# Kernel optimization log

Hardware: AMD Instinct MI355X
Metric: run time of the kernel (lower is better)

Reference implementation:

```python
import jax, jax.numpy as jnp
import numpy as np

N_HEADS = 4
N_NODES = 10000
EMB = 128
N_BATCH = 4096
N_NEAREST = 8
N_SENTINELS = 8


def setup_inputs() -> dict:
    key = jax.random.key(0)
    k1, k2, k3, k4 = jax.random.split(key, 4)
    embeds = jax.random.normal(k1, (N_HEADS, N_NODES, EMB), jnp.float32)
    field = jax.random.uniform(k3, (N_HEADS, N_NODES, EMB), dtype=jnp.float32)
    uncertainty = jnp.ones((1, 1, 1), jnp.float32) * 5.0
    adj = (jax.random.uniform(k4, (N_NODES, N_NODES)) < 0.001).astype(jnp.float32)
    batch_edges = jax.random.randint(k2, (2, N_BATCH), 0, N_NODES)
    return {"embeds": embeds, "field": field, "uncertainty": uncertainty,
            "adj": adj, "batch_edges": batch_edges}


def _knn_samples(embeds, nodes, k):
    # embeds: (h, n, d); nodes: (b,) -> indices of k nearest neighbors, excluding self.
    # Squared L2 distance is monotone in L2 norm, so top-k order matches the
    # original's .norm(dim=3).topk(..., largest=False).
    x = embeds[:, nodes]                                  # (h, b, d)
    x2 = jnp.sum(x * x, axis=-1)[:, :, None]              # (h, b, 1)
    y2 = jnp.sum(embeds * embeds, axis=-1)[:, None, :]    # (h, 1, n)
    d2 = x2 + y2 - 2.0 * jnp.einsum('hbd,hnd->hbn', x, embeds)  # (h, b, n)
    _, idx = jax.lax.top_k(-d2, k + 1)                    # nearest first
    return jax.lax.stop_gradient(idx[:, :, 1:])           # drop self -> (h, b, k)


def reference(embeds, field, uncertainty, adj, batch_edges):
    src, dst = batch_edges[0], batch_edges[1]
    h_idx = jnp.arange(N_HEADS)[:, None, None]

    def build(nodes, nodes_logits, adj_gather):
        samples = _knn_samples(embeds, nodes, N_NEAREST)                 # (h,b,k)
        diff = embeds[:, nodes][:, :, None, :] - embeds[h_idx, samples]  # (h,b,k,d)
        label = uncertainty * (adj_gather(samples) * 2.0 - 1.0)          # (h,b,k)
        g = field[:, nodes_logits]                                        # (h,b,d)
        logits = jnp.einsum('hbkd,hbd->hbk', diff, g) + label
        return logits, diff

    src_logits, src_diff = build(src, dst, lambda s: adj[s, dst[None, :, None]])
    tgt_logits, tgt_diff = build(dst, src, lambda s: adj[src[None, :, None], s])

    logits = jnp.concatenate([src_logits, tgt_logits], axis=2)           # (h,b,2k)
    dist = jnp.linalg.norm(jnp.concatenate([src_diff, tgt_diff], axis=2), axis=3)

    h, b = logits.shape[0], logits.shape[1]
    logits = jnp.concatenate(
        [logits, jnp.zeros((h, b, N_SENTINELS), logits.dtype)], axis=2)
    dist = jnp.concatenate(
        [dist, jnp.ones((h, b, N_SENTINELS), dist.dtype)], axis=2)

    # softmin: softmax(1 - dist)-weighted sum of logits, then mean over heads
    softmin = jnp.sum(logits * jax.nn.softmax(1.0 - dist, axis=2), axis=2)  # (h,b)
    return jax.nn.sigmoid(softmin.mean(axis=0)).reshape(-1)                 # (b,)
```

## Files before the change

kernel.cpp:

```cpp
#include <hip/hip_runtime.h>
#include <math.h>
#include <stdint.h>

#define N_HEADS 4
#define N_NODES 10000
#define NPAD 10112
#define NPG (NPAD / 32)
#define EMB 128
#define N_BATCH 4096
#define NQ (2 * N_BATCH)
#define K 8
#define TQ 32
#define TN 128
#define NTILES (NPAD / TN)
#define PH 2
#define CAP 41
#define WIN 0.5f

typedef __attribute__((ext_vector_type(8))) __bf16 bf16x8;
typedef __attribute__((ext_vector_type(8))) unsigned short ushortx8;
typedef __attribute__((ext_vector_type(16))) float floatx16;

__device__ __forceinline__ unsigned short f2bf(float x) {
  unsigned u = __float_as_uint(x);
  u += 0x7fff + ((u >> 16) & 1);
  return (unsigned short)(u >> 16);
}
__device__ __forceinline__ uint32_t bfup(float f) {
  uint32_t u = __float_as_uint(f);
  return (f >= 0.f) ? ((u + 0xFFFFu) >> 16) : (u >> 16);
}

__device__ __forceinline__ void insert8(float* bs, int* bi, float s, int node) {
  if (s < bs[K - 1]) {
    #pragma unroll
    for (int k2 = K - 1; k2 >= 0; --k2) {
      if (!(s < bs[k2])) break;
      if (k2 < K - 1) { bs[k2 + 1] = bs[k2]; bi[k2 + 1] = bi[k2]; }
      bs[k2] = s; bi[k2] = node;
    }
  }
}

__device__ __forceinline__ size_t pchunk(int g, int c, int lm) {
  return (size_t)g * 4096 + (size_t)(c >> 1) * 512 + (size_t)(c & 1) * 256 + lm * 8;
}

__global__ __launch_bounds__(256) void prep_kernel(
    const float* __restrict__ E, unsigned short* __restrict__ EhiP,
    float* __restrict__ y2g) {
  __shared__ float s_p[8][33];
  const int h = blockIdx.y, g = blockIdx.x;
  const int lm = threadIdx.x & 31, c8 = threadIdx.x >> 5;
  const int n = g * 32 + lm;
  float x[16];
  #pragma unroll
  for (int j = 0; j < 16; ++j) x[j] = 0.f;
  if (n < N_NODES) {
    const float* src = E + (size_t)(h * N_NODES + n) * EMB + c8 * 16;
    #pragma unroll
    for (int j = 0; j < 4; ++j) {
      float4 v = *(const float4*)(src + j * 4);
      x[j * 4 + 0] = v.x; x[j * 4 + 1] = v.y; x[j * 4 + 2] = v.z; x[j * 4 + 3] = v.w;
    }
  }
  float part = 0.f;
  ushortx8 hi[2];
  #pragma unroll
  for (int j = 0; j < 16; ++j) {
    part += x[j] * x[j];
    hi[j >> 3][j & 7] = f2bf(x[j]);
  }
  size_t base = (size_t)h * NPG * 4096;
  #pragma unroll
  for (int lh = 0; lh < 2; ++lh)
    *(ushortx8*)&EhiP[base + pchunk(g, c8 * 2 + lh, lm)] = hi[lh];
  s_p[c8][lm] = part;
  __syncthreads();
  if (threadIdx.x < 32) {
    int nn = g * 32 + threadIdx.x;
    float s = 0.f;
    #pragma unroll
    for (int j = 0; j < 8; ++j) s += s_p[j][threadIdx.x];
    y2g[h * NPAD + nn] = (nn < N_NODES) ? s : 1e30f;
  }
}

__global__ __launch_bounds__(256, 4) void knn_kernel(
    const unsigned short* __restrict__ EhiP, const float* __restrict__ y2g,
    const float* __restrict__ Ef, const int* __restrict__ be,
    int* __restrict__ samples) {
  __shared__ __align__(16) float s_x[TQ * TN];
  __shared__ __align__(16) unsigned short s_ahi[TQ * EMB];
  __shared__ float s_t8S[TQ * 9];
  __shared__ int   s_t8I[TQ * 9];
  __shared__ float s_lsS[TQ * CAP];
  __shared__ int   s_lsI[TQ * CAP];
  __shared__ float s_thr[TQ];
  __shared__ int   s_cnt[TQ];

  const int id = blockIdx.x;
  const int h = (id & 7) >> 1;
  const int qt = ((id >> 3) << 1) | (id & 1);
  const int tid = threadIdx.x;
  const int lane = tid & 63;
  const int w1 = tid >> 6;
  const int lm = lane & 31, lh = lane >> 5;
  const unsigned short* EhiH = EhiP + (size_t)h * NPG * 4096;
  const float* y2H = y2g + h * NPAD;
  const float* EH = Ef + (size_t)h * N_NODES * EMB;

  {
    int r = tid >> 3, cb = (tid & 7) * 2;
    int rx15 = r & 15;
    int q = be[qt * TQ + r];
    int gq = q >> 5, lmq = q & 31;
    #pragma unroll
    for (int c = 0; c < 2; ++c) {
      int lc = cb + c;
      *(bf16x8*)&s_ahi[r * EMB + (lc ^ rx15) * 8] =
          *(const bf16x8*)&EhiH[pchunk(gq, lc, lmq)];
    }
    __syncthreads();
  }

  const int qsel = tid >> 3;
  const int csel = tid & 7;
  const int myq = be[qt * TQ + qsel];
  float bs[K]; int bi[K];
  #pragma unroll
  for (int k2 = 0; k2 < K; ++k2) { bs[k2] = 1e30f; bi[k2] = 0x7fffffff; }
  if (tid < TQ) s_cnt[tid] = 0;

  const int bnode = 32 * w1 + lm;
  const int arx = lm & 15;
  const unsigned short* bhp = EhiH + (size_t)w1 * 4096 + lane * 8;

  #pragma unroll 1
  for (int t = 0; t < PH; ++t) {
    const size_t goff = (size_t)t * 16384;
    float ny = y2H[t * TN + bnode];
    floatx16 acc = {0.f, 0.f, 0.f, 0.f, 0.f, 0.f, 0.f, 0.f,
                    0.f, 0.f, 0.f, 0.f, 0.f, 0.f, 0.f, 0.f};
    #pragma unroll
    for (int ks = 0; ks < 8; ++ks) {
      bf16x8 va = *(const bf16x8*)&s_ahi[lm * EMB + (((ks * 2 + lh) ^ arx)) * 8];
      bf16x8 vbh = *(const bf16x8*)(bhp + goff + ks * 512);
      acc = __builtin_amdgcn_mfma_f32_32x32x16_bf16(va, vbh, acc, 0, 0, 0);
    }
    #pragma unroll
    for (int r = 0; r < 16; ++r) {
      int row = (r & 3) + 8 * (r >> 2) + 4 * lh;
      s_x[row * TN + bnode] = fmaf(-2.f, acc[r], ny);
    }
    __syncthreads();
    int nbp = t * TN;
    #pragma unroll
    for (int s = 0; s < 16; ++s) {
      int j = csel * 16 + ((s + qsel) & 15);
      float sc = s_x[qsel * TN + j];
      int node = nbp + j;
      if (node != myq) insert8(bs, bi, sc, node);
    }
    __syncthreads();
  }

  {
    float* scrS = (float*)s_x;
    int*   scrI = (int*)s_x + TQ * 64;
    #pragma unroll
    for (int k2 = 0; k2 < K; ++k2) {
      scrS[tid * 8 + k2] = bs[k2]; scrI[tid * 8 + k2] = bi[k2];
    }
    __syncthreads();
    if (tid < TQ) {
      int q = tid;
      float ts[K]; int ti[K];
      #pragma unroll
      for (int k2 = 0; k2 < K; ++k2) { ts[k2] = 1e30f; ti[k2] = 0x7fffffff; }
      for (int kk = 0; kk < 64; ++kk) {
        int e = (kk + q) & 63;
        insert8(ts, ti, scrS[q * 64 + e], scrI[q * 64 + e]);
      }
      float thr = ts[K - 1], win = thr + WIN;
      int nc = 0;
      for (int kk = 0; kk < 64; ++kk) {
        int e = (kk + q) & 63;
        float sv = scrS[q * 64 + e]; int iv = scrI[q * 64 + e];
        if (sv <= win && nc < CAP) {
          bool dup = false;
          #pragma unroll
          for (int j = 0; j < K; ++j) dup = dup || (ti[j] == iv);
          if (!dup) { s_lsS[q * CAP + nc] = sv; s_lsI[q * CAP + nc] = iv; ++nc; }
        }
      }
      s_cnt[q] = nc;
      s_thr[q] = win;
      #pragma unroll
      for (int k2 = 0; k2 < K; ++k2) { s_t8S[q * 9 + k2] = ts[k2]; s_t8I[q * 9 + k2] = ti[k2]; }
    }
    __syncthreads();
  }

  uint32_t thrp[8];
  #pragma unroll
  for (int j = 0; j < 8; ++j) {
    int r0 = 2 * j, r1 = 2 * j + 1;
    float t0 = s_thr[(r0 & 3) + 8 * (r0 >> 2) + 4 * lh];
    float t1 = s_thr[(r1 & 3) + 8 * (r1 >> 2) + 4 * lh];
    thrp[j] = bfup(t0) | (bfup(t1) << 16);
  }

  #pragma unroll 1
  for (int t = PH; t < NTILES; ++t) {
    if (t == 4 || t == 8 || t == 16 || t == 32) {
      __syncthreads();
      if (tid < TQ) {
        int q = tid;
        int myqm = be[qt * TQ + q];
        float ts[K]; int ti[K];
        #pragma unroll
        for (int k2 = 0; k2 < K; ++k2) { ts[k2] = s_t8S[q * 9 + k2]; ti[k2] = s_t8I[q * 9 + k2]; }
        int cnt = s_cnt[q]; if (cnt > CAP) cnt = CAP;
        for (int p = 0; p < cnt; ++p) {
          int iv = s_lsI[q * CAP + p];
          if (iv != myqm) insert8(ts, ti, s_lsS[q * CAP + p], iv);
        }
        float thr = ts[K - 1], win = thr + WIN;
        int nc = 0;
        for (int p = 0; p < cnt; ++p) {
          float sv = s_lsS[q * CAP + p]; int iv = s_lsI[q * CAP + p];
          if (sv <= win && iv != myqm) {
            bool dup = false;
            #pragma unroll
            for (int j = 0; j < K; ++j) dup = dup || (ti[j] == iv);
            if (!dup && nc < CAP) { s_lsS[q * CAP + nc] = sv; s_lsI[q * CAP + nc] = iv; ++nc; }
          }
        }
        #pragma unroll
        for (int k2 = 0; k2 < K; ++k2) {
          float sv = s_t8S[q * 9 + k2]; int iv = s_t8I[q * 9 + k2];
          if (sv <= win && iv != myqm && nc < CAP) {
            bool dup = false;
            #pragma unroll
            for (int j = 0; j < K; ++j) dup = dup || (ti[j] == iv);
            if (!dup) { s_lsS[q * CAP + nc] = sv; s_lsI[q * CAP + nc] = iv; ++nc; }
          }
        }
        s_cnt[q] = nc;
        s_thr[q] = win;
        #pragma unroll
        for (int k2 = 0; k2 < K; ++k2) { s_t8S[q * 9 + k2] = ts[k2]; s_t8I[q * 9 + k2] = ti[k2]; }
      }
      __syncthreads();
      #pragma unroll
      for (int j = 0; j < 8; ++j) {
        int r0 = 2 * j, r1 = 2 * j + 1;
        float t0 = s_thr[(r0 & 3) + 8 * (r0 >> 2) + 4 * lh];
        float t1 = s_thr[(r1 & 3) + 8 * (r1 >> 2) + 4 * lh];
        thrp[j] = bfup(t0) | (bfup(t1) << 16);
      }
    }

    const size_t goff = (size_t)t * 16384;
    float ny = y2H[t * TN + bnode];
    floatx16 acc = {0.f, 0.f, 0.f, 0.f, 0.f, 0.f, 0.f, 0.f,
                    0.f, 0.f, 0.f, 0.f, 0.f, 0.f, 0.f, 0.f};
    #pragma unroll
    for (int ks = 0; ks < 8; ++ks) {
      bf16x8 va = *(const bf16x8*)&s_ahi[lm * EMB + (((ks * 2 + lh) ^ arx)) * 8];
      bf16x8 vbh = *(const bf16x8*)(bhp + goff + ks * 512);
      acc = __builtin_amdgcn_mfma_f32_32x32x16_bf16(va, vbh, acc, 0, 0, 0);
    }
    const int node = t * TN + bnode;
    #pragma unroll
    for (int r = 0; r < 16; ++r) {
      float sc = fmaf(-2.f, acc[r], ny);
      float th = (r & 1) ? __uint_as_float(thrp[r >> 1] & 0xFFFF0000u)
                         : __uint_as_float(thrp[r >> 1] << 16);
      if (sc < th) {
        int q = (r & 3) + 8 * (r >> 2) + 4 * lh;
        int p = atomicAdd(&s_cnt[q], 1);
        if (p < CAP) { s_lsS[q * CAP + p] = sc; s_lsI[q * CAP + p] = node; }
      }
    }
  }

  __syncthreads();
  {
    int q = tid >> 3, k = tid & 7;
    int qn = be[qt * TQ + q];
    const float4* Eq = (const float4*)(EH + (size_t)qn * EMB);
    int iv = s_t8I[q * 9 + k];
    if (iv < N_NODES) {
      const float4* En = (const float4*)(EH + (size_t)iv * EMB);
      float d0 = 0.f, d1 = 0.f, d2 = 0.f, d3 = 0.f;
      #pragma unroll
      for (int d = 0; d < 32; ++d) {
        float4 a = Eq[d], b = En[d];
        d0 += a.x * b.x; d1 += a.y * b.y; d2 += a.z * b.z; d3 += a.w * b.w;
      }
      s_t8S[q * 9 + k] = y2H[iv] - 2.f * ((d0 + d1) + (d2 + d3));
    }
    int cnt = s_cnt[q]; if (cnt > CAP) cnt = CAP;
    for (int p = k; p < cnt; p += 8) {
      int jv = s_lsI[q * CAP + p];
      if (jv < N_NODES && jv != qn) {
        const float4* En = (const float4*)(EH + (size_t)jv * EMB);
        float d0 = 0.f, d1 = 0.f, d2 = 0.f, d3 = 0.f;
        #pragma unroll
        for (int d = 0; d < 32; ++d) {
          float4 a = Eq[d], b = En[d];
          d0 += a.x * b.x; d1 += a.y * b.y; d2 += a.z * b.z; d3 += a.w * b.w;
        }
        s_lsS[q * CAP + p] = y2H[jv] - 2.f * ((d0 + d1) + (d2 + d3));
      }
    }
  }
  __syncthreads();
  if (tid < TQ) {
    int q = tid;
    int myqm = be[qt * TQ + q];
    float ts[K]; int ti[K];
    #pragma unroll
    for (int k2 = 0; k2 < K; ++k2) { ts[k2] = 1e30f; ti[k2] = 0x7fffffff; }
    #pragma unroll
    for (int k2 = 0; k2 < K; ++k2)
      insert8(ts, ti, s_t8S[q * 9 + k2], s_t8I[q * 9 + k2]);
    int cnt = s_cnt[q]; if (cnt > CAP) cnt = CAP;
    for (int p = 0; p < cnt; ++p) {
      int iv = s_lsI[q * CAP + p];
      if (iv != myqm) insert8(ts, ti, s_lsS[q * CAP + p], iv);
    }
    size_t base = ((size_t)h * NQ + qt * TQ + q) * K;
    #pragma unroll
    for (int k2 = 0; k2 < K; ++k2) samples[base + k2] = ti[k2];
  }
}

__global__ __launch_bounds__(256) void predict_kernel(
    const float* __restrict__ E, const float* __restrict__ F,
    const float* __restrict__ unc, const float* __restrict__ adj,
    const int* __restrict__ be, const int* __restrict__ samples,
    float* __restrict__ out) {
  int b = blockIdx.x;
  int h = threadIdx.x >> 6;
  int lane = threadIdx.x & 63;
  __shared__ float smv[N_HEADS];

  int srcb = be[b];
  int dstb = be[N_BATCH + b];
  const float* Eh = E + (size_t)h * N_NODES * EMB;
  const float* Fh = F + (size_t)h * N_NODES * EMB;
  float2 es = *(const float2*)(Eh + (size_t)srcb * EMB + 2 * lane);
  float2 ed = *(const float2*)(Eh + (size_t)dstb * EMB + 2 * lane);
  float2 fs = *(const float2*)(Fh + (size_t)srcb * EMB + 2 * lane);
  float2 fd = *(const float2*)(Fh + (size_t)dstb * EMB + 2 * lane);
  float u = unc[0];

  float logit[16], dist[16];
  #pragma unroll
  for (int j = 0; j < 16; ++j) {
    bool isrc = (j < 8);
    int qrow = isrc ? b : (N_BATCH + b);
    int s = samples[((size_t)h * NQ + qrow) * K + (j & 7)];
    float2 ev = *(const float2*)(Eh + (size_t)s * EMB + 2 * lane);
    float2 bb = isrc ? es : ed;
    float2 g = isrc ? fd : fs;
    float dx = bb.x - ev.x, dy = bb.y - ev.y;
    float dot = dx * g.x + dy * g.y;
    float nrm = dx * dx + dy * dy;
    #pragma unroll
    for (int o = 32; o > 0; o >>= 1) {
      dot += __shfl_xor(dot, o);
      nrm += __shfl_xor(nrm, o);
    }
    float a = isrc ? adj[(size_t)s * N_NODES + dstb]
                   : adj[(size_t)srcb * N_NODES + s];
    logit[j] = dot + u * (2.0f * a - 1.0f);
    dist[j] = sqrtf(nrm);
  }

  float m = 0.0f;
  #pragma unroll
  for (int j = 0; j < 16; ++j) m = fmaxf(m, 1.0f - dist[j]);
  float Z = 8.0f * expf(-m);
  float num = 0.0f;
  #pragma unroll
  for (int j = 0; j < 16; ++j) {
    float e = expf(1.0f - dist[j] - m);
    Z += e;
    num += logit[j] * e;
  }
  if (lane == 0) smv[h] = num / Z;
  __syncthreads();
  if (threadIdx.x == 0) {
    float t = 0.25f * (smv[0] + smv[1] + smv[2] + smv[3]);
    out[b] = 1.0f / (1.0f + expf(-t));
  }
}

extern "C" void kernel_launch(void* const* d_in, const int* in_sizes, int n_in,
                              void* d_out, int out_size, void* d_ws,
                              size_t ws_size, hipStream_t stream) {
  const float* E = (const float*)d_in[0];
  const float* F = (const float*)d_in[1];
  const float* U = (const float*)d_in[2];
  const float* A = (const float*)d_in[3];
  const int* be = (const int*)d_in[4];
  float* out = (float*)d_out;

  char* w = (char*)d_ws;
  unsigned short* EhiP = (unsigned short*)(w);
  float* y2g = (float*)(w + 10354688);
  int* samples = (int*)(w + 10516736);

  prep_kernel<<<dim3(NPG, N_HEADS), 256, 0, stream>>>(E, EhiP, y2g);
  knn_kernel<<<dim3((NQ / TQ) * N_HEADS), 256, 0, stream>>>(EhiP, y2g, E, be, samples);
  predict_kernel<<<dim3(N_BATCH), 256, 0, stream>>>(E, F, U, A, be, samples, out);
}
```

Measured before the change: 779.9 us.

## Double query tile per block, keep A fragments in registers, add early-skip filter

Raises the query tile from 32 to 64 so each streamed B fragment of the embedding matrix feeds two MFMAs, halving global traffic for the node embeddings per query. Query A fragments are held in registers instead of LDS, and a per-lane min-vs-max-threshold test skips the per-row candidate insertion loop when no score can qualify. Occupancy is pinned to 2 waves per EU to fit the larger register footprint, and the grid halves, which may reduce parallelism and latency hiding. The phase-1 and rescoring thread mappings are adjusted to the 64-query tile.

After: 809.7 us. 3.8% more time.

```diff
diff --git a/kernel.cpp b/kernel.cpp
--- a/kernel.cpp
+++ b/kernel.cpp
@@ -10,7 +10,7 @@
 #define N_BATCH 4096
 #define NQ (2 * N_BATCH)
 #define K 8
-#define TQ 32
+#define TQ 64
 #define TN 128
 #define NTILES (NPAD / TN)
 #define PH 2
@@ -86,12 +86,13 @@
   }
 }
 
-__global__ __launch_bounds__(256, 4) void knn_kernel(
+__global__ __launch_bounds__(256)
+__attribute__((amdgpu_waves_per_eu(2, 2)))
+void knn_kernel(
     const unsigned short* __restrict__ EhiP, const float* __restrict__ y2g,
     const float* __restrict__ Ef, const int* __restrict__ be,
     int* __restrict__ samples) {
   __shared__ __align__(16) float s_x[TQ * TN];
-  __shared__ __align__(16) unsigned short s_ahi[TQ * EMB];
   __shared__ float s_t8S[TQ * 9];
   __shared__ int   s_t8I[TQ * 9];
   __shared__ float s_lsS[TQ * CAP];
@@ -110,22 +111,21 @@
   const float* y2H = y2g + h * NPAD;
   const float* EH = Ef + (size_t)h * N_NODES * EMB;
 
+  bf16x8 a0[8], a1[8];
   {
-    int r = tid >> 3, cb = (tid & 7) * 2;
-    int rx15 = r & 15;
-    int q = be[qt * TQ + r];
-    int gq = q >> 5, lmq = q & 31;
-    #pragma unroll
-    for (int c = 0; c < 2; ++c) {
-      int lc = cb + c;
-      *(bf16x8*)&s_ahi[r * EMB + (lc ^ rx15) * 8] =
-          *(const bf16x8*)&EhiH[pchunk(gq, lc, lmq)];
-    }
-    __syncthreads();
-  }
-
-  const int qsel = tid >> 3;
-  const int csel = tid & 7;
+    int q0 = be[qt * TQ + lm];
+    int q1 = be[qt * TQ + 32 + lm];
+    int g0 = q0 >> 5, l0 = q0 & 31;
+    int g1 = q1 >> 5, l1 = q1 & 31;
+    #pragma unroll
+    for (int ks = 0; ks < 8; ++ks) {
+      a0[ks] = *(const bf16x8*)&EhiH[pchunk(g0, ks * 2 + lh, l0)];
+      a1[ks] = *(const bf16x8*)&EhiH[pchunk(g1, ks * 2 + lh, l1)];
+    }
+  }
+
+  const int qsel = tid >> 2;
+  const int csel = tid & 3;
   const int myq = be[qt * TQ + qsel];
   float bs[K]; int bi[K];
   #pragma unroll
@@ -133,31 +133,32 @@
   if (tid < TQ) s_cnt[tid] = 0;
 
   const int bnode = 32 * w1 + lm;
-  const int arx = lm & 15;
   const unsigned short* bhp = EhiH + (size_t)w1 * 4096 + lane * 8;
 
   #pragma unroll 1
   for (int t = 0; t < PH; ++t) {
     const size_t goff = (size_t)t * 16384;
     float ny = y2H[t * TN + bnode];
-    floatx16 acc = {0.f, 0.f, 0.f, 0.f, 0.f, 0.f, 0.f, 0.f,
-                    0.f, 0.f, 0.f, 0.f, 0.f, 0.f, 0.f, 0.f};
+    floatx16 acc0 = {0.f, 0.f, 0.f, 0.f, 0.f, 0.f, 0.f, 0.f,
+                     0.f, 0.f, 0.f, 0.f, 0.f, 0.f, 0.f, 0.f};
+    floatx16 acc1 = acc0;
     #pragma unroll
     for (int ks = 0; ks < 8; ++ks) {
-      bf16x8 va = *(const bf16x8*)&s_ahi[lm * EMB + (((ks * 2 + lh) ^ arx)) * 8];
       bf16x8 vbh = *(const bf16x8*)(bhp + goff + ks * 512);
-      acc = __builtin_amdgcn_mfma_f32_32x32x16_bf16(va, vbh, acc, 0, 0, 0);
+      acc0 = __builtin_amdgcn_mfma_f32_32x32x16_bf16(a0[ks], vbh, acc0, 0, 0, 0);
+      acc1 = __builtin_amdgcn_mfma_f32_32x32x16_bf16(a1[ks], vbh, acc1, 0, 0, 0);
     }
     #pragma unroll
     for (int r = 0; r < 16; ++r) {
       int row = (r & 3) + 8 * (r >> 2) + 4 * lh;
-      s_x[row * TN + bnode] = fmaf(-2.f, acc[r], ny);
+      s_x[row * TN + bnode] = fmaf(-2.f, acc0[r], ny);
+      s_x[(row + 32) * TN + bnode] = fmaf(-2.f, acc1[r], ny);
     }
     __syncthreads();
     int nbp = t * TN;
     #pragma unroll
-    for (int s = 0; s < 16; ++s) {
-      int j = csel * 16 + ((s + qsel) & 15);
+    for (int s = 0; s < 32; ++s) {
+      int j = csel * 32 + ((s + qsel) & 31);
       float sc = s_x[qsel * TN + j];
       int node = nbp + j;
       if (node != myq) insert8(bs, bi, sc, node);
@@ -167,7 +168,7 @@
 
   {
     float* scrS = (float*)s_x;
-    int*   scrI = (int*)s_x + TQ * 64;
+    int*   scrI = (int*)s_x + TQ * 32;
     #pragma unroll
     for (int k2 = 0; k2 < K; ++k2) {
       scrS[tid * 8 + k2] = bs[k2]; scrI[tid * 8 + k2] = bi[k2];
@@ -178,15 +179,15 @@
       float ts[K]; int ti[K];
       #pragma unroll
       for (int k2 = 0; k2 < K; ++k2) { ts[k2] = 1e30f; ti[k2] = 0x7fffffff; }
-      for (int kk = 0; kk < 64; ++kk) {
-        int e = (kk + q) & 63;
-        insert8(ts, ti, scrS[q * 64 + e], scrI[q * 64 + e]);
+      for (int kk = 0; kk < 32; ++kk) {
+        int e = (kk + q) & 31;
+        insert8(ts, ti, scrS[q * 32 + e], scrI[q * 32 + e]);
       }
       float thr = ts[K - 1], win = thr + WIN;
       int nc = 0;
-      for (int kk = 0; kk < 64; ++kk) {
-        int e = (kk + q) & 63;
-        float sv = scrS[q * 64 + e]; int iv = scrI[q * 64 + e];
+      for (int kk = 0; kk < 32; ++kk) {
+        int e = (kk + q) & 31;
+        float sv = scrS[q * 32 + e]; int iv = scrI[q * 32 + e];
         if (sv <= win && nc < CAP) {
           bool dup = false;
           #pragma unroll
@@ -202,13 +203,22 @@
     __syncthreads();
   }
 
-  uint32_t thrp[8];
-  #pragma unroll
-  for (int j = 0; j < 8; ++j) {
-    int r0 = 2 * j, r1 = 2 * j + 1;
-    float t0 = s_thr[(r0 & 3) + 8 * (r0 >> 2) + 4 * lh];
-    float t1 = s_thr[(r1 & 3) + 8 * (r1 >> 2) + 4 * lh];
-    thrp[j] = bfup(t0) | (bfup(t1) << 16);
+  uint32_t thrp0[8], thrp1[8];
+  float thmax0, thmax1;
+  {
+    thmax0 = -1e30f; thmax1 = -1e30f;
+    #pragma unroll
+    for (int j = 0; j < 8; ++j) {
+      int r0 = 2 * j, r1 = 2 * j + 1;
+      int w0 = (r0 & 3) + 8 * (r0 >> 2) + 4 * lh;
+      int w1r = (r1 & 3) + 8 * (r1 >> 2) + 4 * lh;
+      float t00 = s_thr[w0], t01 = s_thr[w1r];
+      float t10 = s_thr[w0 + 32], t11 = s_thr[w1r + 32];
+      thrp0[j] = bfup(t00) | (bfup(t01) << 16);
+      thrp1[j] = bfup(t10) | (bfup(t11) << 16);
+      thmax0 = fmaxf(thmax0, fmaxf(t00, t01));
+      thmax1 = fmaxf(thmax1, fmaxf(t10, t11));
+    }
   }
 
   #pragma unroll 1
@@ -253,57 +263,98 @@
         for (int k2 = 0; k2 < K; ++k2) { s_t8S[q * 9 + k2] = ts[k2]; s_t8I[q * 9 + k2] = ti[k2]; }
       }
       __syncthreads();
+      thmax0 = -1e30f; thmax1 = -1e30f;
       #pragma unroll
       for (int j = 0; j < 8; ++j) {
         int r0 = 2 * j, r1 = 2 * j + 1;
-        float t0 = s_thr[(r0 & 3) + 8 * (r0 >> 2) + 4 * lh];
-        float t1 = s_thr[(r1 & 3) + 8 * (r1 >> 2) + 4 * lh];
-        thrp[j] = bfup(t0) | (bfup(t1) << 16);
+        int w0 = (r0 & 3) + 8 * (r0 >> 2) + 4 * lh;
+        int w1r = (r1 & 3) + 8 * (r1 >> 2) + 4 * lh;
+        float t00 = s_thr[w0], t01 = s_thr[w1r];
+        float t10 = s_thr[w0 + 32], t11 = s_thr[w1r + 32];
+        thrp0[j] = bfup(t00) | (bfup(t01) << 16);
+        thrp1[j] = bfup(t10) | (bfup(t11) << 16);
+        thmax0 = fmaxf(thmax0, fmaxf(t00, t01));
+        thmax1 = fmaxf(thmax1, fmaxf(t10, t11));
       }
     }
 
     const size_t goff = (size_t)t * 16384;
     float ny = y2H[t * TN + bnode];
-    floatx16 acc = {0.f, 0.f, 0.f, 0.f, 0.f, 0.f, 0.f, 0.f,
-                    0.f, 0.f, 0.f, 0.f, 0.f, 0.f, 0.f, 0.f};
+    floatx16 acc0 = {0.f, 0.f, 0.f, 0.f, 0.f, 0.f, 0.f, 0.f,
+                     0.f, 0.f, 0.f, 0.f, 0.f, 0.f, 0.f, 0.f};
+    floatx16 acc1 = acc0;
     #pragma unroll
     for (int ks = 0; ks < 8; ++ks) {
-      bf16x8 va = *(const bf16x8*)&s_ahi[lm * EMB + (((ks * 2 + lh) ^ arx)) * 8];
       bf16x8 vbh = *(const bf16x8*)(bhp + goff + ks * 512);
-      acc = __builtin_amdgcn_mfma_f32_32x32x16_bf16(va, vbh, acc, 0, 0, 0);
+      acc0 = __builtin_amdgcn_mfma_f32_32x32x16_bf16(a0[ks], vbh, acc0, 0, 0, 0);
+      acc1 = __builtin_amdgcn_mfma_f32_32x32x16_bf16(a1[ks], vbh, acc1, 0, 0, 0);
     }
     const int node = t * TN + bnode;
-    #pragma unroll
-    for (int r = 0; r < 16; ++r) {
-      float sc = fmaf(-2.f, acc[r], ny);
-      float th = (r & 1) ? __uint_as_float(thrp[r >> 1] & 0xFFFF0000u)
-                         : __uint_as_float(thrp[r >> 1] << 16);
-      if (sc < th) {
-        int q = (r & 3) + 8 * (r >> 2) + 4 * lh;
-        int p = atomicAdd(&s_cnt[q], 1);
-        if (p < CAP) { s_lsS[q * CAP + p] = sc; s_lsI[q * CAP + p] = node; }
+
+    {
+      float sc[16];
+      #pragma unroll
+      for (int r = 0; r < 16; ++r) sc[r] = fmaf(-2.f, acc0[r], ny);
+      float mn = sc[0];
+      #pragma unroll
+      for (int r = 1; r < 16; ++r) mn = fminf(mn, sc[r]);
+      if (mn < thmax0) {
+        #pragma unroll
+        for (int r = 0; r < 16; ++r) {
+          float th = (r & 1) ? __uint_as_float(thrp0[r >> 1] & 0xFFFF0000u)
+                             : __uint_as_float(thrp0[r >> 1] << 16);
+          if (sc[r] < th) {
+            int q = (r & 3) + 8 * (r >> 2) + 4 * lh;
+            int p = atomicAdd(&s_cnt[q], 1);
+            if (p < CAP) { s_lsS[q * CAP + p] = sc[r]; s_lsI[q * CAP + p] = node; }
+          }
+        }
+      }
+    }
+    {
+      float sc[16];
+      #pragma unroll
+      for (int r = 0; r < 16; ++r) sc[r] = fmaf(-2.f, acc1[r], ny);
+      float mn = sc[0];
+      #pragma unroll
+      for (int r = 1; r < 16; ++r) mn = fminf(mn, sc[r]);
+      if (mn < thmax1) {
+        #pragma unroll
+        for (int r = 0; r < 16; ++r) {
+          float th = (r & 1) ? __uint_as_float(thrp1[r >> 1] & 0xFFFF0000u)
+                             : __uint_as_float(thrp1[r >> 1] << 16);
+          if (sc[r] < th) {
+            int q = 32 + (r & 3) + 8 * (r >> 2) + 4 * lh;
+            int p = atomicAdd(&s_cnt[q], 1);
+            if (p < CAP) { s_lsS[q * CAP + p] = sc[r]; s_lsI[q * CAP + p] = node; }
+          }
+        }
       }
     }
   }
 
   __syncthreads();
   {
-    int q = tid >> 3, k = tid & 7;
+    int q = tid >> 2, k4 = tid & 3;
     int qn = be[qt * TQ + q];
     const float4* Eq = (const float4*)(EH + (size_t)qn * EMB);
-    int iv = s_t8I[q * 9 + k];
-    if (iv < N_NODES) {
-      const float4* En = (const float4*)(EH + (size_t)iv * EMB);
-      float d0 = 0.f, d1 = 0.f, d2 = 0.f, d3 = 0.f;
-      #pragma unroll
-      for (int d = 0; d < 32; ++d) {
-        float4 a = Eq[d], b = En[d];
-        d0 += a.x * b.x; d1 += a.y * b.y; d2 += a.z * b.z; d3 += a.w * b.w;
-      }
-      s_t8S[q * 9 + k] = y2H[iv] - 2.f * ((d0 + d1) + (d2 + d3));
+    #pragma unroll
+    for (int kk = 0; kk < 2; ++kk) {
+      int k = k4 + kk * 4;
+      int iv = s_t8I[q * 9 + k];
+      if (iv < N_NODES) {
+        const float4* En = (const float4*)(EH + (size_t)iv * EMB);
+        float d0 = 0.f, d1 = 0.f, d2 = 0.f, d3 = 0.f;
+        #pragma unroll
+        for (int d = 0; d < 32; ++d) {
+          float4 a = Eq[d], b = En[d];
+          d0 += a.x * b.x; d1 += a.y * b.y; d2 += a.z * b.z; d3 += a.w * b.w;
+        }
+        s_t8S[q * 9 + k] = y2H[iv] - 2.f * ((d0 + d1) + (d2 + d3));
+      }
     }
     int cnt = s_cnt[q]; if (cnt > CAP) cnt = CAP;
-    for (int p = k; p < cnt; p += 8) {
+    for (int p = k4; p < cnt; p += 4) {
       int jv = s_lsI[q * CAP + p];
       if (jv < N_NODES && jv != qn) {
         const float4* En = (const float4*)(EH + (size_t)jv * EMB);
```

## Double query tile to 64 per block and keep query fragments in registers

Applied to the files above, without the earlier changes.

Each knn block now handles 64 queries with 512 threads: two row-groups of 4 waves share the same node tile, so each loaded B fragment from global memory serves twice as many queries. The query A-operand fragments are loaded once into registers instead of being staged in shared memory and reread every tile. The warm-up phase and the initial candidate merge are split into two halves so the existing 32-row shared scratch can be reused. The candidate cap drops from 41 to 32 and extra threshold refresh points are added, which raises the risk of candidate-list overflow and changes occupancy because of more registers and larger blocks.

New measurement: 842.3 us. 1.08x slower.

```diff
diff --git a/kernel.cpp b/kernel.cpp
--- a/kernel.cpp
+++ b/kernel.cpp
@@ -10,11 +10,11 @@
 #define N_BATCH 4096
 #define NQ (2 * N_BATCH)
 #define K 8
-#define TQ 32
+#define TQ 64
 #define TN 128
 #define NTILES (NPAD / TN)
 #define PH 2
-#define CAP 41
+#define CAP 32
 #define WIN 0.5f
 
 typedef __attribute__((ext_vector_type(8))) __bf16 bf16x8;
@@ -86,12 +86,11 @@
   }
 }
 
-__global__ __launch_bounds__(256, 4) void knn_kernel(
+__global__ __launch_bounds__(512, 4) void knn_kernel(
     const unsigned short* __restrict__ EhiP, const float* __restrict__ y2g,
     const float* __restrict__ Ef, const int* __restrict__ be,
     int* __restrict__ samples) {
-  __shared__ __align__(16) float s_x[TQ * TN];
-  __shared__ __align__(16) unsigned short s_ahi[TQ * EMB];
+  __shared__ __align__(16) float s_x[32 * TN];
   __shared__ float s_t8S[TQ * 9];
   __shared__ int   s_t8I[TQ * 9];
   __shared__ float s_lsS[TQ * CAP];
@@ -104,24 +103,21 @@
   const int qt = ((id >> 3) << 1) | (id & 1);
   const int tid = threadIdx.x;
   const int lane = tid & 63;
-  const int w1 = tid >> 6;
+  const int w = tid >> 6;
+  const int rb = w >> 2;
+  const int grp = w & 3;
   const int lm = lane & 31, lh = lane >> 5;
   const unsigned short* EhiH = EhiP + (size_t)h * NPG * 4096;
   const float* y2H = y2g + h * NPAD;
   const float* EH = Ef + (size_t)h * N_NODES * EMB;
 
+  bf16x8 a[8];
   {
-    int r = tid >> 3, cb = (tid & 7) * 2;
-    int rx15 = r & 15;
-    int q = be[qt * TQ + r];
-    int gq = q >> 5, lmq = q & 31;
-    #pragma unroll
-    for (int c = 0; c < 2; ++c) {
-      int lc = cb + c;
-      *(bf16x8*)&s_ahi[r * EMB + (lc ^ rx15) * 8] =
-          *(const bf16x8*)&EhiH[pchunk(gq, lc, lmq)];
-    }
-    __syncthreads();
+    int q0 = be[qt * TQ + rb * 32 + lm];
+    int g0 = q0 >> 5, l0 = q0 & 31;
+    #pragma unroll
+    for (int ks = 0; ks < 8; ++ks)
+      a[ks] = *(const bf16x8*)&EhiH[pchunk(g0, ks * 2 + lh, l0)];
   }
 
   const int qsel = tid >> 3;
@@ -132,9 +128,8 @@
   for (int k2 = 0; k2 < K; ++k2) { bs[k2] = 1e30f; bi[k2] = 0x7fffffff; }
   if (tid < TQ) s_cnt[tid] = 0;
 
-  const int bnode = 32 * w1 + lm;
-  const int arx = lm & 15;
-  const unsigned short* bhp = EhiH + (size_t)w1 * 4096 + lane * 8;
+  const int bnode = 32 * grp + lm;
+  const unsigned short* bhp = EhiH + (size_t)grp * 4096 + lane * 8;
 
   #pragma unroll 1
   for (int t = 0; t < PH; ++t) {
@@ -144,76 +139,102 @@
                     0.f, 0.f, 0.f, 0.f, 0.f, 0.f, 0.f, 0.f};
     #pragma unroll
     for (int ks = 0; ks < 8; ++ks) {
-      bf16x8 va = *(const bf16x8*)&s_ahi[lm * EMB + (((ks * 2 + lh) ^ arx)) * 8];
       bf16x8 vbh = *(const bf16x8*)(bhp + goff + ks * 512);
-      acc = __builtin_amdgcn_mfma_f32_32x32x16_bf16(va, vbh, acc, 0, 0, 0);
-    }
-    #pragma unroll
-    for (int r = 0; r < 16; ++r) {
-      int row = (r & 3) + 8 * (r >> 2) + 4 * lh;
-      s_x[row * TN + bnode] = fmaf(-2.f, acc[r], ny);
+      acc = __builtin_amdgcn_mfma_f32_32x32x16_bf16(a[ks], vbh, acc, 0, 0, 0);
+    }
+    if (rb == 0) {
+      #pragma unroll
+      for (int r = 0; r < 16; ++r) {
+        int row = (r & 3) + 8 * (r >> 2) + 4 * lh;
+        s_x[row * TN + bnode] = fmaf(-2.f, acc[r], ny);
+      }
     }
     __syncthreads();
-    int nbp = t * TN;
-    #pragma unroll
-    for (int s = 0; s < 16; ++s) {
-      int j = csel * 16 + ((s + qsel) & 15);
-      float sc = s_x[qsel * TN + j];
-      int node = nbp + j;
-      if (node != myq) insert8(bs, bi, sc, node);
+    if (qsel < 32) {
+      #pragma unroll
+      for (int s = 0; s < 16; ++s) {
+        int j = csel * 16 + ((s + qsel) & 15);
+        float sc = s_x[qsel * TN + j];
+        int node = t * TN + j;
+        if (node != myq) insert8(bs, bi, sc, node);
+      }
+    }
+    __syncthreads();
+    if (rb == 1) {
+      #pragma unroll
+      for (int r = 0; r < 16; ++r) {
+        int row = (r & 3) + 8 * (r >> 2) + 4 * lh;
+        s_x[row * TN + bnode] = fmaf(-2.f, acc[r], ny);
+      }
+    }
+    __syncthreads();
+    if (qsel >= 32) {
+      #pragma unroll
+      for (int s = 0; s < 16; ++s) {
+        int j = csel * 16 + ((s + qsel) & 15);
+        float sc = s_x[(qsel - 32) * TN + j];
+        int node = t * TN + j;
+        if (node != myq) insert8(bs, bi, sc, node);
+      }
     }
     __syncthreads();
   }
 
   {
     float* scrS = (float*)s_x;
-    int*   scrI = (int*)s_x + TQ * 64;
-    #pragma unroll
-    for (int k2 = 0; k2 < K; ++k2) {
-      scrS[tid * 8 + k2] = bs[k2]; scrI[tid * 8 + k2] = bi[k2];
-    }
-    __syncthreads();
-    if (tid < TQ) {
-      int q = tid;
-      float ts[K]; int ti[K];
-      #pragma unroll
-      for (int k2 = 0; k2 < K; ++k2) { ts[k2] = 1e30f; ti[k2] = 0x7fffffff; }
-      for (int kk = 0; kk < 64; ++kk) {
-        int e = (kk + q) & 63;
-        insert8(ts, ti, scrS[q * 64 + e], scrI[q * 64 + e]);
-      }
-      float thr = ts[K - 1], win = thr + WIN;
-      int nc = 0;
-      for (int kk = 0; kk < 64; ++kk) {
-        int e = (kk + q) & 63;
-        float sv = scrS[q * 64 + e]; int iv = scrI[q * 64 + e];
-        if (sv <= win && nc < CAP) {
-          bool dup = false;
-          #pragma unroll
-          for (int j = 0; j < K; ++j) dup = dup || (ti[j] == iv);
-          if (!dup) { s_lsS[q * CAP + nc] = sv; s_lsI[q * CAP + nc] = iv; ++nc; }
-        }
-      }
-      s_cnt[q] = nc;
-      s_thr[q] = win;
-      #pragma unroll
-      for (int k2 = 0; k2 < K; ++k2) { s_t8S[q * 9 + k2] = ts[k2]; s_t8I[q * 9 + k2] = ti[k2]; }
-    }
-    __syncthreads();
+    int*   scrI = (int*)s_x + 2048;
+    #pragma unroll 1
+    for (int ph = 0; ph < 2; ++ph) {
+      if ((tid >> 8) == ph) {
+        int lt = tid & 255;
+        #pragma unroll
+        for (int k2 = 0; k2 < K; ++k2) {
+          scrS[lt * 8 + k2] = bs[k2]; scrI[lt * 8 + k2] = bi[k2];
+        }
+      }
+      __syncthreads();
+      if (tid < 32) {
+        int q = ph * 32 + tid;
+        float ts[K]; int ti[K];
+        #pragma unroll
+        for (int k2 = 0; k2 < K; ++k2) { ts[k2] = 1e30f; ti[k2] = 0x7fffffff; }
+        for (int kk = 0; kk < 64; ++kk) {
+          int e = (kk + q) & 63;
+          insert8(ts, ti, scrS[tid * 64 + e], scrI[tid * 64 + e]);
+        }
+        float thr = ts[K - 1], win = thr + WIN;
+        int nc = 0;
+        for (int kk = 0; kk < 64; ++kk) {
+          int e = (kk + q) & 63;
+          float sv = scrS[tid * 64 + e]; int iv = scrI[tid * 64 + e];
+          if (sv <= win && nc < CAP) {
+            bool dup = false;
+            #pragma unroll
+            for (int j = 0; j < K; ++j) dup = dup || (ti[j] == iv);
+            if (!dup) { s_lsS[q * CAP + nc] = sv; s_lsI[q * CAP + nc] = iv; ++nc; }
+          }
+        }
+        s_cnt[q] = nc;
+        s_thr[q] = win;
+        #pragma unroll
+        for (int k2 = 0; k2 < K; ++k2) { s_t8S[q * 9 + k2] = ts[k2]; s_t8I[q * 9 + k2] = ti[k2]; }
+      }
+      __syncthreads();
+    }
   }
 
   uint32_t thrp[8];
   #pragma unroll
   for (int j = 0; j < 8; ++j) {
     int r0 = 2 * j, r1 = 2 * j + 1;
-    float t0 = s_thr[(r0 & 3) + 8 * (r0 >> 2) + 4 * lh];
-    float t1 = s_thr[(r1 & 3) + 8 * (r1 >> 2) + 4 * lh];
-    thrp[j] = bfup(t0) | (bfup(t1) << 16);
+    int w0 = (r0 & 3) + 8 * (r0 >> 2) + 4 * lh;
+    int w1r = (r1 & 3) + 8 * (r1 >> 2) + 4 * lh;
+    thrp[j] = bfup(s_thr[rb * 32 + w0]) | (bfup(s_thr[rb * 32 + w1r]) << 16);
   }
 
   #pragma unroll 1
   for (int t = PH; t < NTILES; ++t) {
-    if (t == 4 || t == 8 || t == 16 || t == 32) {
+    if (t == 4 || t == 8 || t == 16 || t == 32 || t == 48 || t == 64) {
       __syncthreads();
       if (tid < TQ) {
         int q = tid;
@@ -256,9 +277,9 @@
       #pragma unroll
       for (int j = 0; j < 8; ++j) {
         int r0 = 2 * j, r1 = 2 * j + 1;
-        float t0 = s_thr[(r0 & 3) + 8 * (r0 >> 2) + 4 * lh];
-        float t1 = s_thr[(r1 & 3) + 8 * (r1 >> 2) + 4 * lh];
-        thrp[j] = bfup(t0) | (bfup(t1) << 16);
+        int w0 = (r0 & 3) + 8 * (r0 >> 2) + 4 * lh;
+        int w1r = (r1 & 3) + 8 * (r1 >> 2) + 4 * lh;
+        thrp[j] = bfup(s_thr[rb * 32 + w0]) | (bfup(s_thr[rb * 32 + w1r]) << 16);
       }
     }
 
@@ -268,9 +289,8 @@
                     0.f, 0.f, 0.f, 0.f, 0.f, 0.f, 0.f, 0.f};
     #pragma unroll
     for (int ks = 0; ks < 8; ++ks) {
-      bf16x8 va = *(const bf16x8*)&s_ahi[lm * EMB + (((ks * 2 + lh) ^ arx)) * 8];
       bf16x8 vbh = *(const bf16x8*)(bhp + goff + ks * 512);
-      acc = __builtin_amdgcn_mfma_f32_32x32x16_bf16(va, vbh, acc, 0, 0, 0);
+      acc = __builtin_amdgcn_mfma_f32_32x32x16_bf16(a[ks], vbh, acc, 0, 0, 0);
     }
     const int node = t * TN + bnode;
     #pragma unroll
@@ -279,7 +299,7 @@
       float th = (r & 1) ? __uint_as_float(thrp[r >> 1] & 0xFFFF0000u)
                          : __uint_as_float(thrp[r >> 1] << 16);
       if (sc < th) {
-        int q = (r & 3) + 8 * (r >> 2) + 4 * lh;
+        int q = rb * 32 + (r & 3) + 8 * (r >> 2) + 4 * lh;
         int p = atomicAdd(&s_cnt[q], 1);
         if (p < CAP) { s_lsS[q * CAP + p] = sc; s_lsI[q * CAP + p] = node; }
       }
@@ -297,8 +317,8 @@
       float d0 = 0.f, d1 = 0.f, d2 = 0.f, d3 = 0.f;
       #pragma unroll
       for (int d = 0; d < 32; ++d) {
-        float4 a = Eq[d], b = En[d];
-        d0 += a.x * b.x; d1 += a.y * b.y; d2 += a.z * b.z; d3 += a.w * b.w;
+        float4 a2 = Eq[d], b = En[d];
+        d0 += a2.x * b.x; d1 += a2.y * b.y; d2 += a2.z * b.z; d3 += a2.w * b.w;
       }
       s_t8S[q * 9 + k] = y2H[iv] - 2.f * ((d0 + d1) + (d2 + d3));
     }
@@ -310,8 +330,8 @@
         float d0 = 0.f, d1 = 0.f, d2 = 0.f, d3 = 0.f;
         #pragma unroll
         for (int d = 0; d < 32; ++d) {
-          float4 a = Eq[d], b = En[d];
-          d0 += a.x * b.x; d1 += a.y * b.y; d2 += a.z * b.z; d3 += a.w * b.w;
+          float4 a2 = Eq[d], b = En[d];
+          d0 += a2.x * b.x; d1 += a2.y * b.y; d2 += a2.z * b.z; d3 += a2.w * b.w;
         }
         s_lsS[q * CAP + p] = y2H[jv] - 2.f * ((d0 + d1) + (d2 + d3));
       }
@@ -416,6 +436,6 @@
   int* samples = (int*)(w + 10516736);
 
   prep_kernel<<<dim3(NPG, N_HEADS), 256, 0, stream>>>(E, EhiP, y2g);
-  knn_kernel<<<dim3((NQ / TQ) * N_HEADS), 256, 0, stream>>>(EhiP, y2g, E, be, samples);
+  knn_kernel<<<dim3((NQ / TQ) * N_HEADS), 512, 0, stream>>>(EhiP, y2g, E, be, samples);
   predict_kernel<<<dim3(N_BATCH), 256, 0, stream>>>(E, F, U, A, be, samples, out);
 }
```
